# Kernel optimization log

Measured on AMD Instinct MI355X. Metric: run time of the kernel, lower is better.

## Reference

```python
import jax, jax.numpy as jnp
import numpy as np
from jax import lax

D = 512      # inter_dim
E = 768      # expand_dim
S = 256      # squeeze_dim
BUCKET = 64
N_BLOCK = 6

def layernorm(x, g, b, eps):
    m = jnp.mean(x, axis=-1, keepdims=True)
    v = jnp.mean(jnp.square(x - m), axis=-1, keepdims=True)
    return (x - m) / jnp.sqrt(v + eps) * g + b

def setup_inputs():
    key = jax.random.key(0)
    ks = jax.random.split(key, 12)
    B, N, IN = 4, 4096, 768
    def rn(k, shape, scale):
        return jax.random.normal(k, shape, dtype=jnp.float32) * scale
    return {
        "xs": jax.random.normal(ks[0], (B, N, IN), dtype=jnp.float32),
        # in1: Linear(IN, D) + LayerNorm(eps=1e-8) + LeakyReLU(0.1)
        "W_in": rn(ks[1], (IN, D), IN ** -0.5), "b_in": jnp.zeros(D),
        "ln_in_g": jnp.ones(D), "ln_in_b": jnp.zeros(D),
        # 6 GAU (FlashQuadAttention) blocks, params stacked on leading axis
        "blk_ln_g": jnp.ones((N_BLOCK, D)), "blk_ln_b": jnp.zeros((N_BLOCK, D)),
        "blk_Wuv": rn(ks[2], (N_BLOCK, D, 2 * E + S), D ** -0.5),
        "blk_buv": jnp.zeros((N_BLOCK, 2 * E + S)),
        "blk_gamma": jnp.ones((N_BLOCK, 2, S)) + rn(ks[3], (N_BLOCK, 2, S), 0.02),
        "blk_beta": rn(ks[4], (N_BLOCK, 2, S), 0.02),
        "blk_Wo": rn(ks[5], (N_BLOCK, E, D), E ** -0.5),
        "blk_bo": jnp.zeros((N_BLOCK, D)),
        # tr_layer (applied inside tree loop)
        "tr_W": rn(ks[6], (D, D), D ** -0.5), "tr_b": jnp.zeros(D),
        "tr_a": jnp.full((), 1e-6, dtype=jnp.float32),
        # out1 = TransLayer + Linear(D, out_dim)
        "tr2_W": rn(ks[7], (D, D), D ** -0.5), "tr2_b": jnp.zeros(D),
        "tr2_a": jnp.full((), 1e-6, dtype=jnp.float32),
        "out_W": rn(ks[8], (D, 2), D ** -0.5), "out_b": jnp.zeros(2),
    }

def reference(xs, W_in, b_in, ln_in_g, ln_in_b,
              blk_ln_g, blk_ln_b, blk_Wuv, blk_buv, blk_gamma, blk_beta,
              blk_Wo, blk_bo, tr_W, tr_b, tr_a, tr2_W, tr2_b, tr2_a,
              out_W, out_b):
    def subnet(h):  # h: [n_buckets, BUCKET, D]
        def step(h, p):
            lg, lb, Wuv, buv, gam, bet, Wo, bo = p
            n = layernorm(h, lg, lb, 1e-5)
            uvb = jax.nn.silu(n @ Wuv + buv)
            u, v, base = uvb[..., :E], uvb[..., E:2 * E], uvb[..., 2 * E:]
            q = base * gam[0] + bet[0]
            k = base * gam[1] + bet[1]
            Lq = h.shape[1]
            a = jnp.square(jax.nn.relu(jnp.einsum('gls,gms->glm', q, k) / Lq))
            o = jnp.einsum('glm,gme->gle', a, v) * u
            return h + o @ Wo + bo, None
        h, _ = lax.scan(step, h, (blk_ln_g, blk_ln_b, blk_Wuv, blk_buv,
                                  blk_gamma, blk_beta, blk_Wo, blk_bo))
        return h

    def tr_layer(x, W, b, a):
        return x + jax.nn.gelu(x @ W + b, approximate=False) * a

    def run_sample(x):  # x: [N, in_dim]
        h = layernorm(x @ W_in + b_in, ln_in_g, ln_in_b, 1e-8)
        h = jnp.where(h > 0, h, 0.1 * h)  # LeakyReLU(0.1)
        seq = h
        ys = []
        while seq.shape[0] > 1:  # static shapes -> unrolled tree levels
            ids = jnp.argsort(jnp.linalg.norm(seq, axis=-1))  # sort by L2 norm
            buckets = seq[ids].reshape(-1, BUCKET, D)
            gy = subnet(buckets).mean(axis=1)           # [n_buckets, D]
            ys.append(tr_layer(gy, tr_W, tr_b, tr_a).mean(axis=0))
            seq = gy
        return jnp.stack(ys, 0).mean(0)  # [D]

    y = jax.vmap(run_sample)(xs)          # [B, D]
    y = tr_layer(y, tr2_W, tr2_b, tr2_a)  # out1 TransLayer
    return y @ out_W + out_b              # [B, out_dim]
```

## Files before the change

### kernel.cpp

```cpp
#include <hip/hip_runtime.h>
#include <math.h>

#define R1C 16384

enum { OP_STORE = 0, OP_SILU = 1, OP_RESID = 2, OP_TR = 3 };

typedef _Float16 f16x8 __attribute__((ext_vector_type(8)));
typedef float f32x4 __attribute__((ext_vector_type(4)));

__device__ __forceinline__ float silu_f(float x) { return x / (1.0f + __expf(-x)); }
__device__ __forceinline__ float gelu_f(float x) {
  return 0.5f * x * (1.0f + erff(x * 0.70710678118654752f));
}

__device__ __forceinline__ void gll16(const void* g, const void* l) {
  __builtin_amdgcn_global_load_lds(
      (const __attribute__((address_space(1))) unsigned int*)g,
      (__attribute__((address_space(3))) unsigned int*)l, 16, 0, 0);
}


__global__ __launch_bounds__(256) void gemm_f16(
    const _Float16* __restrict__ A, int lda,
    const _Float16* __restrict__ Bt, int ldb,
    float* __restrict__ C, int ldc, int K,
    const float* __restrict__ bias, int mode,
    const int* __restrict__ ids)
{
  const int BUF = 128 * 32;
  __shared__ _Float16 As[2 * BUF];
  __shared__ _Float16 Bs[2 * BUF];
  int tid = threadIdx.x;
  int lane = tid & 63, w = tid >> 6;
  int wm = w >> 1, wn = w & 1;
  int row0 = blockIdx.y * 128, col0 = blockIdx.x * 128;

  int p0 = w * 64 + lane;
  int p1 = 256 + w * 64 + lane;
  int m0 = p0 >> 2, k0e = (((p0 & 3) - (m0 >> 1)) & 3) * 8;
  int m1 = p1 >> 2, k1e = (((p1 & 3) - (m1 >> 1)) & 3) * 8;
  const _Float16* gA0 = A + (size_t)(row0 + m0) * lda + k0e;
  const _Float16* gA1 = A + (size_t)(row0 + m1) * lda + k1e;
  const _Float16* gB0 = Bt + (size_t)(col0 + m0) * ldb + k0e;
  const _Float16* gB1 = Bt + (size_t)(col0 + m1) * ldb + k1e;
  const _Float16* lA0 = As + (size_t)(w * 64) * 8;
  const _Float16* lA1 = As + (size_t)(256 + w * 64) * 8;
  const _Float16* lB0 = Bs + (size_t)(w * 64) * 8;
  const _Float16* lB1 = Bs + (size_t)(256 + w * 64) * 8;

  int mrow = lane & 15, quad = lane >> 4;
  const f16x8* aptr[4];
  const f16x8* bptr[4];
#pragma unroll
  for (int t = 0; t < 4; ++t) {
    int ml = wm * 64 + t * 16 + mrow;
    aptr[t] = (const f16x8*)(As + (size_t)(ml * 4 + ((quad + (ml >> 1)) & 3)) * 8);
    int nl = wn * 64 + t * 16 + mrow;
    bptr[t] = (const f16x8*)(Bs + (size_t)(nl * 4 + ((quad + (nl >> 1)) & 3)) * 8);
  }

  f32x4 acc[4][4] = {};

  gll16(gA0, lA0); gll16(gA1, lA1);
  gll16(gB0, lB0); gll16(gB1, lB1);
  gA0 += 32; gA1 += 32; gB0 += 32; gB1 += 32;

  for (int kt = 0; kt < K; kt += 32) {
    int cur = (kt >> 5) & 1;
    __syncthreads();
    if (kt + 32 < K) {
      int nx = cur ^ 1;
      gll16(gA0, lA0 + nx * BUF); gll16(gA1, lA1 + nx * BUF);
      gll16(gB0, lB0 + nx * BUF); gll16(gB1, lB1 + nx * BUF);
      gA0 += 32; gA1 += 32; gB0 += 32; gB1 += 32;
    }
    int fo = cur * (BUF / 8);
    f16x8 af[4], bfr[4];
#pragma unroll
    for (int t = 0; t < 4; ++t) { af[t] = *(aptr[t] + fo); bfr[t] = *(bptr[t] + fo); }
#pragma unroll
    for (int mt = 0; mt < 4; ++mt)
#pragma unroll
      for (int nt = 0; nt < 4; ++nt)
        acc[mt][nt] = __builtin_amdgcn_mfma_f32_16x16x32_f16(
            af[mt], bfr[nt], acc[mt][nt], 0, 0, 0);
  }

#pragma unroll
  for (int mt = 0; mt < 4; ++mt) {
#pragma unroll
    for (int nt = 0; nt < 4; ++nt) {
      int c = col0 + wn * 64 + nt * 16 + mrow;
      float bv = bias ? bias[c] : 0.0f;
#pragma unroll
      for (int reg = 0; reg < 4; ++reg) {
        int r = row0 + wm * 64 + mt * 16 + quad * 4 + reg;
        float val = acc[mt][nt][reg] + bv;
        if (mode == OP_STORE) {
          C[(size_t)r * ldc + c] = val;
        } else if (mode == OP_SILU) {
          C[(size_t)r * ldc + c] = silu_f(val);
        } else {
          int hr = ids ? ids[r] : r;
          C[(size_t)hr * ldc + c] += val;
        }
      }
    }
  }
}

__global__ __launch_bounds__(256) void gemm_f16_split(
    const _Float16* __restrict__ Ah, const _Float16* __restrict__ Al, int lda,
    const _Float16* __restrict__ Bh, const _Float16* __restrict__ Bl, int ldb,
    float* __restrict__ C, int ldc, int K, const float* __restrict__ bias)
{
  const int BUF = 128 * 32;
  __shared__ _Float16 AsH[2 * BUF], AsL[2 * BUF];
  __shared__ _Float16 BsH[2 * BUF], BsL[2 * BUF];
  int tid = threadIdx.x;
  int lane = tid & 63, w = tid >> 6;
  int wm = w >> 1, wn = w & 1;
  int row0 = blockIdx.y * 128, col0 = blockIdx.x * 128;

  int p0 = w * 64 + lane;
  int p1 = 256 + w * 64 + lane;
  int m0 = p0 >> 2, k0e = (((p0 & 3) - (m0 >> 1)) & 3) * 8;
  int m1 = p1 >> 2, k1e = (((p1 & 3) - (m1 >> 1)) & 3) * 8;
  size_t a0 = (size_t)(row0 + m0) * lda + k0e;
  size_t a1 = (size_t)(row0 + m1) * lda + k1e;
  size_t b0 = (size_t)(col0 + m0) * ldb + k0e;
  size_t b1 = (size_t)(col0 + m1) * ldb + k1e;
  size_t l0 = (size_t)(w * 64) * 8;
  size_t l1 = (size_t)(256 + w * 64) * 8;

  int mrow = lane & 15, quad = lane >> 4;
  size_t aoff[4], boff[4];
#pragma unroll
  for (int t = 0; t < 4; ++t) {
    int ml = wm * 64 + t * 16 + mrow;
    aoff[t] = (size_t)(ml * 4 + ((quad + (ml >> 1)) & 3)) * 8;
    int nl = wn * 64 + t * 16 + mrow;
    boff[t] = (size_t)(nl * 4 + ((quad + (nl >> 1)) & 3)) * 8;
  }

  f32x4 acc[4][4] = {};

  gll16(Ah + a0, AsH + l0); gll16(Ah + a1, AsH + l1);
  gll16(Al + a0, AsL + l0); gll16(Al + a1, AsL + l1);
  gll16(Bh + b0, BsH + l0); gll16(Bh + b1, BsH + l1);
  gll16(Bl + b0, BsL + l0); gll16(Bl + b1, BsL + l1);
  a0 += 32; a1 += 32; b0 += 32; b1 += 32;

  for (int kt = 0; kt < K; kt += 32) {
    int cur = (kt >> 5) & 1;
    __syncthreads();
    if (kt + 32 < K) {
      int nx = cur ^ 1;
      size_t o = (size_t)nx * BUF;
      gll16(Ah + a0, AsH + l0 + o); gll16(Ah + a1, AsH + l1 + o);
      gll16(Al + a0, AsL + l0 + o); gll16(Al + a1, AsL + l1 + o);
      gll16(Bh + b0, BsH + l0 + o); gll16(Bh + b1, BsH + l1 + o);
      gll16(Bl + b0, BsL + l0 + o); gll16(Bl + b1, BsL + l1 + o);
      a0 += 32; a1 += 32; b0 += 32; b1 += 32;
    }
    size_t o = (size_t)cur * BUF;
    f16x8 ah[4], al_[4], bh[4], bl[4];
#pragma unroll
    for (int t = 0; t < 4; ++t) {
      ah[t]  = *(const f16x8*)(AsH + aoff[t] + o);
      al_[t] = *(const f16x8*)(AsL + aoff[t] + o);
      bh[t]  = *(const f16x8*)(BsH + boff[t] + o);
      bl[t]  = *(const f16x8*)(BsL + boff[t] + o);
    }
#pragma unroll
    for (int mt = 0; mt < 4; ++mt)
#pragma unroll
      for (int nt = 0; nt < 4; ++nt) {
        acc[mt][nt] = __builtin_amdgcn_mfma_f32_16x16x32_f16(
            ah[mt], bh[nt], acc[mt][nt], 0, 0, 0);
        acc[mt][nt] = __builtin_amdgcn_mfma_f32_16x16x32_f16(
            ah[mt], bl[nt], acc[mt][nt], 0, 0, 0);
        acc[mt][nt] = __builtin_amdgcn_mfma_f32_16x16x32_f16(
            al_[mt], bh[nt], acc[mt][nt], 0, 0, 0);
      }
  }

#pragma unroll
  for (int mt = 0; mt < 4; ++mt)
#pragma unroll
    for (int nt = 0; nt < 4; ++nt) {
      int c = col0 + wn * 64 + nt * 16 + mrow;
      float bv = bias ? bias[c] : 0.0f;
#pragma unroll
      for (int reg = 0; reg < 4; ++reg) {
        int r = row0 + wm * 64 + mt * 16 + quad * 4 + reg;
        C[(size_t)r * ldc + c] = acc[mt][nt][reg] + bv;
      }
    }
}

__global__ __launch_bounds__(256) void gemm_f16_uvb(
    const _Float16* __restrict__ A, int lda,
    const _Float16* __restrict__ Bt,
    int c0, int nu,
    _Float16* __restrict__ ub, _Float16* __restrict__ vb, float* __restrict__ baseb,
    int CH, int K, const float* __restrict__ buv)
{
  const int BUF = 128 * 32;
  __shared__ _Float16 As[2 * BUF];
  __shared__ _Float16 Bs[2 * BUF];
  int tid = threadIdx.x;
  int lane = tid & 63, w = tid >> 6;
  int wm = w >> 1, wn = w & 1;
  int row0 = blockIdx.y * 128;

  int x = blockIdx.x;
  int xl, regbase, ldc_, is_base = 0;
  _Float16* dst16 = nullptr;
  if (x < nu)            { xl = x;          regbase = c0;        dst16 = ub; ldc_ = CH; }
  else if (x < 2 * nu)   { xl = x - nu;     regbase = 768 + c0;  dst16 = vb; ldc_ = CH; }
  else                   { xl = x - 2 * nu; regbase = 1536;      is_base = 1; ldc_ = 256; }
  int brow0 = regbase + xl * 128;
  int dcol0 = xl * 128;

  int p0 = w * 64 + lane;
  int p1 = 256 + w * 64 + lane;
  int m0 = p0 >> 2, k0e = (((p0 & 3) - (m0 >> 1)) & 3) * 8;
  int m1 = p1 >> 2, k1e = (((p1 & 3) - (m1 >> 1)) & 3) * 8;
  const _Float16* gA0 = A + (size_t)(row0 + m0) * lda + k0e;
  const _Float16* gA1 = A + (size_t)(row0 + m1) * lda + k1e;
  const _Float16* gB0 = Bt + (size_t)(brow0 + m0) * 512 + k0e;
  const _Float16* gB1 = Bt + (size_t)(brow0 + m1) * 512 + k1e;
  const _Float16* lA0 = As + (size_t)(w * 64) * 8;
  const _Float16* lA1 = As + (size_t)(256 + w * 64) * 8;
  const _Float16* lB0 = Bs + (size_t)(w * 64) * 8;
  const _Float16* lB1 = Bs + (size_t)(256 + w * 64) * 8;

  int mrow = lane & 15, quad = lane >> 4;
  const f16x8* aptr[4];
  const f16x8* bptr[4];
#pragma unroll
  for (int t = 0; t < 4; ++t) {
    int ml = wm * 64 + t * 16 + mrow;
    aptr[t] = (const f16x8*)(As + (size_t)(ml * 4 + ((quad + (ml >> 1)) & 3)) * 8);
    int nl = wn * 64 + t * 16 + mrow;
    bptr[t] = (const f16x8*)(Bs + (size_t)(nl * 4 + ((quad + (nl >> 1)) & 3)) * 8);
  }

  f32x4 acc[4][4] = {};

  gll16(gA0, lA0); gll16(gA1, lA1);
  gll16(gB0, lB0); gll16(gB1, lB1);
  gA0 += 32; gA1 += 32; gB0 += 32; gB1 += 32;

  for (int kt = 0; kt < K; kt += 32) {
    int cur = (kt >> 5) & 1;
    __syncthreads();
    if (kt + 32 < K) {
      int nx = cur ^ 1;
      gll16(gA0, lA0 + nx * BUF); gll16(gA1, lA1 + nx * BUF);
      gll16(gB0, lB0 + nx * BUF); gll16(gB1, lB1 + nx * BUF);
      gA0 += 32; gA1 += 32; gB0 += 32; gB1 += 32;
    }
    int fo = cur * (BUF / 8);
    f16x8 af[4], bfr[4];
#pragma unroll
    for (int t = 0; t < 4; ++t) { af[t] = *(aptr[t] + fo); bfr[t] = *(bptr[t] + fo); }
#pragma unroll
    for (int mt = 0; mt < 4; ++mt)
#pragma unroll
      for (int nt = 0; nt < 4; ++nt)
        acc[mt][nt] = __builtin_amdgcn_mfma_f32_16x16x32_f16(
            af[mt], bfr[nt], acc[mt][nt], 0, 0, 0);
  }

#pragma unroll
  for (int mt = 0; mt < 4; ++mt) {
#pragma unroll
    for (int nt = 0; nt < 4; ++nt) {
      int lc = wn * 64 + nt * 16 + mrow;
      float bv = buv[brow0 + lc];
#pragma unroll
      for (int reg = 0; reg < 4; ++reg) {
        int r = row0 + wm * 64 + mt * 16 + quad * 4 + reg;
        float val = silu_f(acc[mt][nt][reg] + bv);
        if (is_base) baseb[(size_t)r * 256 + dcol0 + lc] = val;
        else         dst16[(size_t)r * ldc_ + dcol0 + lc] = (_Float16)val;
      }
    }
  }
}

__global__ __launch_bounds__(256) void attnapply_fused(
    const float* __restrict__ base, const float* __restrict__ gb,
    const float* __restrict__ bb, const _Float16* __restrict__ v,
    const _Float16* __restrict__ u, _Float16* __restrict__ t, int CH)
{
  __shared__ _Float16 smem[3 * 64 * 72];
  _Float16* qs = smem;
  _Float16* ks = smem + 64 * 72;
  _Float16* al = smem + 2 * 64 * 72;
  _Float16* vT = smem;

  int g = blockIdx.x, tid = threadIdx.x;
  int lane = tid & 63, w = tid >> 6;
  int mrow = lane & 15, quad = lane >> 4;
  int srow = tid >> 2, scol = (tid & 3) * 16;

  f32x4 acc[4] = {};
  for (int s0 = 0; s0 < 256; s0 += 64) {
    const float* bp = base + ((size_t)g * 64 + srow) * 256 + s0 + scol;
#pragma unroll
    for (int j4 = 0; j4 < 4; ++j4) {
      float4 xv = *(const float4*)(bp + j4 * 4);
      float xx[4] = {xv.x, xv.y, xv.z, xv.w};
#pragma unroll
      for (int j = 0; j < 4; ++j) {
        int s = s0 + scol + j4 * 4 + j;
        qs[srow * 72 + scol + j4 * 4 + j] = (_Float16)(xx[j] * gb[s] + bb[s]);
        ks[srow * 72 + scol + j4 * 4 + j] = (_Float16)(xx[j] * gb[256 + s] + bb[256 + s]);
      }
    }
    __syncthreads();
#pragma unroll
    for (int ks2 = 0; ks2 < 2; ++ks2) {
      f16x8 aq = *(const f16x8*)(qs + (w * 16 + mrow) * 72 + ks2 * 32 + quad * 8);
#pragma unroll
      for (int nt = 0; nt < 4; ++nt) {
        f16x8 bk = *(const f16x8*)(ks + (nt * 16 + mrow) * 72 + ks2 * 32 + quad * 8);
        acc[nt] = __builtin_amdgcn_mfma_f32_16x16x32_f16(aq, bk, acc[nt], 0, 0, 0);
      }
    }
    __syncthreads();
  }
#pragma unroll
  for (int nt = 0; nt < 4; ++nt)
#pragma unroll
    for (int reg = 0; reg < 4; ++reg) {
      float val = acc[nt][reg] * (1.0f / 64.0f);
      val = val > 0.0f ? val : 0.0f;
      val = val * val;
      al[(w * 16 + quad * 4 + reg) * 72 + nt * 16 + mrow] = (_Float16)val;
    }
  __syncthreads();

  for (int e0 = 0; e0 < CH; e0 += 64) {
    const _Float16* vp = v + ((size_t)g * 64 + srow) * CH + e0 + scol;
    f16x8 x0 = *(const f16x8*)vp;
    f16x8 x1 = *(const f16x8*)(vp + 8);
#pragma unroll
    for (int j = 0; j < 8; ++j) {
      vT[(scol + j) * 72 + srow] = x0[j];
      vT[(scol + 8 + j) * 72 + srow] = x1[j];
    }
    __syncthreads();
    f32x4 acc2[4] = {};
#pragma unroll
    for (int ks2 = 0; ks2 < 2; ++ks2) {
      f16x8 af = *(const f16x8*)(al + (w * 16 + mrow) * 72 + ks2 * 32 + quad * 8);
#pragma unroll
      for (int nt = 0; nt < 4; ++nt) {
        f16x8 bf = *(const f16x8*)(vT + (nt * 16 + mrow) * 72 + ks2 * 32 + quad * 8);
        acc2[nt] = __builtin_amdgcn_mfma_f32_16x16x32_f16(af, bf, acc2[nt], 0, 0, 0);
      }
    }
#pragma unroll
    for (int nt = 0; nt < 4; ++nt)
#pragma unroll
      for (int reg = 0; reg < 4; ++reg) {
        int row = w * 16 + quad * 4 + reg;
        int col = e0 + nt * 16 + mrow;
        size_t idx = ((size_t)g * 64 + row) * CH + col;
        t[idx] = (_Float16)(acc2[nt][reg] * (float)u[idx]);
      }
    __syncthreads();
  }
}

__global__ __launch_bounds__(256) void gemm_f32(
    const float* __restrict__ A, int lda,
    const float* __restrict__ B, int ldb,
    float* __restrict__ C, int ldc,
    int M, int N, int K,
    const float* __restrict__ bias, int mode,
    const int* __restrict__ ids,
    const float* __restrict__ X,
    const float* __restrict__ alpha)
{
  __shared__ float As[16][68];
  __shared__ float Bs[16][68];
  int tid = threadIdx.x;
  int tx = tid & 15, ty = tid >> 4;
  int col0 = blockIdx.x * 64, row0 = blockIdx.y * 64;
  float acc[4][4] = {};
  int arow = tid >> 2;
  int ak   = (tid & 3) * 4;
  int bk   = tid >> 4;
  int bn   = (tid & 15) * 4;

  for (int kt = 0; kt < K; kt += 16) {
    float4 av = make_float4(0.f, 0.f, 0.f, 0.f);
    if (row0 + arow < M)
      av = *(const float4*)&A[(size_t)(row0 + arow) * lda + kt + ak];
    As[ak + 0][arow] = av.x; As[ak + 1][arow] = av.y;
    As[ak + 2][arow] = av.z; As[ak + 3][arow] = av.w;
    float4 bv = *(const float4*)&B[(size_t)(kt + bk) * ldb + col0 + bn];
    *(float4*)&Bs[bk][bn] = bv;
    __syncthreads();
#pragma unroll
    for (int k = 0; k < 16; ++k) {
      const float4 a4 = *(const float4*)&As[k][ty * 4];
      const float4 b4 = *(const float4*)&Bs[k][tx * 4];
      float a_[4] = {a4.x, a4.y, a4.z, a4.w};
      float b_[4] = {b4.x, b4.y, b4.z, b4.w};
#pragma unroll
      for (int i = 0; i < 4; ++i)
#pragma unroll
        for (int j = 0; j < 4; ++j)
          acc[i][j] = fmaf(a_[i], b_[j], acc[i][j]);
    }
    __syncthreads();
  }

#pragma unroll
  for (int i = 0; i < 4; ++i) {
    int r = row0 + ty * 4 + i;
    if (r >= M) continue;
#pragma unroll
    for (int j = 0; j < 4; ++j) {
      int c = col0 + tx * 4 + j;
      float val = acc[i][j] + (bias ? bias[c] : 0.0f);
      if (mode == OP_STORE) {
        C[(size_t)r * ldc + c] = val;
      } else if (mode == OP_SILU) {
        C[(size_t)r * ldc + c] = silu_f(val);
      } else if (mode == OP_RESID) {
        int hr = ids ? ids[r] : r;
        C[(size_t)hr * ldc + c] += val;
      } else {
        C[(size_t)r * ldc + c] = X[(size_t)r * ldc + c] + gelu_f(val) * alpha[0];
      }
    }
  }
}

__global__ __launch_bounds__(256) void transpose_cast(
    const float* __restrict__ in, _Float16* __restrict__ out, int K, int N)
{
  in  += (size_t)blockIdx.z * K * N;
  out += (size_t)blockIdx.z * K * N;
  __shared__ float t[32][33];
  int k0 = blockIdx.y * 32, n0 = blockIdx.x * 32;
  int tx = threadIdx.x & 31, ty = threadIdx.x >> 5;
  for (int i = ty; i < 32; i += 8) {
    int k = k0 + i, n = n0 + tx;
    t[i][tx] = (k < K && n < N) ? in[(size_t)k * N + n] : 0.0f;
  }
  __syncthreads();
  for (int i = ty; i < 32; i += 8) {
    int n = n0 + i, k = k0 + tx;
    if (n < N && k < K) out[(size_t)n * K + k] = (_Float16)t[tx][i];
  }
}

__global__ __launch_bounds__(256) void transpose_split(
    const float* __restrict__ in, _Float16* __restrict__ hi,
    _Float16* __restrict__ lo, int K, int N)
{
  __shared__ float t[32][33];
  int k0 = blockIdx.y * 32, n0 = blockIdx.x * 32;
  int tx = threadIdx.x & 31, ty = threadIdx.x >> 5;
  for (int i = ty; i < 32; i += 8) {
    int k = k0 + i, n = n0 + tx;
    t[i][tx] = (k < K && n < N) ? in[(size_t)k * N + n] : 0.0f;
  }
  __syncthreads();
  for (int i = ty; i < 32; i += 8) {
    int n = n0 + i, k = k0 + tx;
    if (n < N && k < K) {
      float x = t[tx][i];
      _Float16 h = (_Float16)x;
      hi[(size_t)n * K + k] = h;
      lo[(size_t)n * K + k] = (_Float16)(x - (float)h);
    }
  }
}

__global__ __launch_bounds__(256) void split_f16_kernel(
    const float* __restrict__ in, _Float16* __restrict__ hi,
    _Float16* __restrict__ lo, int n)
{
  int i = blockIdx.x * 256 + threadIdx.x;
  if (i < n) {
    float x = in[i];
    _Float16 h = (_Float16)x;
    hi[i] = h;
    lo[i] = (_Float16)(x - (float)h);
  }
}

template <typename OUT>
__global__ __launch_bounds__(256) void ln_kernel(
    const float* __restrict__ src, const int* __restrict__ ids,
    OUT* __restrict__ dst, const float* __restrict__ g,
    const float* __restrict__ b, float eps, int leaky,
    float* __restrict__ nrm2)
{
  int r = blockIdx.x;
  int sr = ids ? ids[r] : r;
  int tid = threadIdx.x;
  float v0 = src[(size_t)sr * 512 + tid];
  float v1 = src[(size_t)sr * 512 + tid + 256];
  __shared__ float red[256], red2[256];
  red[tid] = v0 + v1;
  red2[tid] = v0 * v0 + v1 * v1;
  __syncthreads();
  for (int s = 128; s > 0; s >>= 1) {
    if (tid < s) { red[tid] += red[tid + s]; red2[tid] += red2[tid + s]; }
    __syncthreads();
  }
  float mean = red[0] * (1.0f / 512.0f);
  float var  = red2[0] * (1.0f / 512.0f) - mean * mean;
  float rs = rsqrtf(var + eps);
  float o0 = (v0 - mean) * rs * g[tid] + b[tid];
  float o1 = (v1 - mean) * rs * g[tid + 256] + b[tid + 256];
  if (leaky) {
    o0 = o0 > 0.0f ? o0 : 0.1f * o0;
    o1 = o1 > 0.0f ? o1 : 0.1f * o1;
  }
  dst[(size_t)r * 512 + tid] = (OUT)o0;
  dst[(size_t)r * 512 + tid + 256] = (OUT)o1;
  if (nrm2) {
    __syncthreads();
    red[tid] = o0 * o0 + o1 * o1;
    __syncthreads();
    for (int s = 128; s > 0; s >>= 1) {
      if (tid < s) red[tid] += red[tid + s];
      __syncthreads();
    }
    if (tid == 0) nrm2[r] = red[0];
  }
}

__global__ __launch_bounds__(128) void permute_rows(
    const float* __restrict__ src, const int* __restrict__ ids,
    float* __restrict__ dst)
{
  int r = blockIdx.x, sr = ids[r];
  const float4* s = (const float4*)(src + (size_t)sr * 512);
  float4* d = (float4*)(dst + (size_t)r * 512);
  d[threadIdx.x] = s[threadIdx.x];
}

__global__ __launch_bounds__(1024) void sort_kernel(const float* __restrict__ norm2,
                                                    int* __restrict__ ids)
{
  __shared__ float key[4096];
  __shared__ int   val[4096];
  int s = blockIdx.x, tid = threadIdx.x;
  for (int i = tid; i < 4096; i += 1024) { key[i] = norm2[s * 4096 + i]; val[i] = i; }
  __syncthreads();
  for (int len = 2; len <= 4096; len <<= 1) {
    for (int j = len >> 1; j > 0; j >>= 1) {
      for (int t = tid; t < 2048; t += 1024) {
        int i1 = (t << 1) - (t & (j - 1));
        int i2 = i1 + j;
        bool up = ((i1 & len) == 0);
        float ka = key[i1], kb = key[i2];
        int va = val[i1], vb = val[i2];
        bool gt = (ka > kb) || (ka == kb && va > vb);
        if (gt == up) {
          key[i1] = kb; key[i2] = ka;
          val[i1] = vb; val[i2] = va;
        }
      }
      __syncthreads();
    }
  }
  for (int i = tid; i < 4096; i += 1024) ids[s * 4096 + i] = s * 4096 + val[i];
}

__global__ __launch_bounds__(256) void bucketmean_kernel(
    const float* __restrict__ src, const int* __restrict__ ids,
    float* __restrict__ dst)
{
  int g = blockIdx.x, tid = threadIdx.x;
  float s0 = 0.0f, s1 = 0.0f;
  for (int i = 0; i < 64; ++i) {
    int r = g * 64 + i;
    if (ids) r = ids[r];
    s0 += src[(size_t)r * 512 + tid];
    s1 += src[(size_t)r * 512 + tid + 256];
  }
  dst[(size_t)g * 512 + tid] = s0 * (1.0f / 64.0f);
  dst[(size_t)g * 512 + tid + 256] = s1 * (1.0f / 64.0f);
}

__global__ void avg_kernel(const float* __restrict__ a, const float* __restrict__ b,
                           float* __restrict__ o, int n)
{
  int i = blockIdx.x * 256 + threadIdx.x;
  if (i < n) o[i] = 0.5f * (a[i] + b[i]);
}

__global__ void out_kernel(const float* __restrict__ y, const float* __restrict__ W,
                           const float* __restrict__ b, float* __restrict__ out)
{
  int tid = threadIdx.x;
  if (tid < 8) {
    int s = tid >> 1, j = tid & 1;
    float acc = b[j];
    for (int d = 0; d < 512; ++d) acc += y[s * 512 + d] * W[d * 2 + j];
    out[s * 2 + j] = acc;
  }
}

extern "C" void kernel_launch(void* const* d_in, const int* in_sizes, int n_in,
                              void* d_out, int out_size, void* d_ws, size_t ws_size,
                              hipStream_t stream)
{
  const float* xs       = (const float*)d_in[0];
  const float* W_in     = (const float*)d_in[1];
  const float* b_in     = (const float*)d_in[2];
  const float* ln_in_g  = (const float*)d_in[3];
  const float* ln_in_b  = (const float*)d_in[4];
  const float* blk_ln_g = (const float*)d_in[5];
  const float* blk_ln_b = (const float*)d_in[6];
  const float* blk_Wuv  = (const float*)d_in[7];
  const float* blk_buv  = (const float*)d_in[8];
  const float* blk_gam  = (const float*)d_in[9];
  const float* blk_bet  = (const float*)d_in[10];
  const float* blk_Wo   = (const float*)d_in[11];
  const float* blk_bo   = (const float*)d_in[12];
  const float* tr_W     = (const float*)d_in[13];
  const float* tr_b     = (const float*)d_in[14];
  const float* tr_a     = (const float*)d_in[15];
  const float* tr2_W    = (const float*)d_in[16];
  const float* tr2_b    = (const float*)d_in[17];
  const float* tr2_a    = (const float*)d_in[18];
  const float* out_W    = (const float*)d_in[19];
  const float* out_b    = (const float*)d_in[20];
  float* outp = (float*)d_out;

  const size_t R1 = R1C;

  char* wsb = (char*)d_ws;
  size_t off = 0;
  auto carve = [&](size_t bytes) {
    char* r = wsb + off;
    off = (off + bytes + 255) & ~(size_t)255;
    return (void*)r;
  };
  float* h      = (float*)carve(R1 * 512 * 4);
  float* hslot  = (float*)carve(R1 * 512 * 4);
  float* norm2b = (float*)carve(R1 * 4);
  int*   idsb   = (int*)carve(R1 * 4);
  float* gy     = (float*)carve((size_t)256 * 512 * 4);
  float* tl     = (float*)carve((size_t)256 * 512 * 4);
  float* gy2    = (float*)carve(4 * 512 * 4);
  float* ys0    = (float*)carve(4 * 512 * 4);
  float* ys1    = (float*)carve(4 * 512 * 4);
  float* yv     = (float*)carve(4 * 512 * 4);
  float* y2     = (float*)carve(4 * 512 * 4);
  _Float16* Wuvt = (_Float16*)carve((size_t)6 * 1792 * 512 * 2);
  _Float16* Wot  = (_Float16*)carve((size_t)6 * 512 * 768 * 2);
  size_t persistent = off;

  size_t stageA_sorted = 2 * R1 * 768 * 2 + 2 * (size_t)512 * 768 * 2 + R1 * 512 * 4 + 2048;
  size_t block768 = R1 * 256 * 4 + 3 * R1 * (size_t)768 * 2 + 2048;
  size_t un_sorted = stageA_sorted > block768 ? stageA_sorted : block768;
  bool sorted_mode = (persistent + un_sorted + 4096 <= ws_size);

  int CH = 768;
  bool splitA = true;
  if (!sorted_mode) {
    size_t stageA_fb = 2 * R1 * 768 * 2 + 2 * (size_t)512 * 768 * 2 + 1024;
    auto block_bytes = [&](size_t ch) {
      return R1 * 256 * 4 + 3 * R1 * ch * 2 + 2048;
    };
    CH = 0; splitA = false;
    const int cand[4] = {768, 384, 256, 128};
    for (int ci = 0; ci < 4; ++ci) {
      size_t bb2 = block_bytes(cand[ci]);
      size_t un2 = bb2 > stageA_fb ? bb2 : stageA_fb;
      if (persistent + un2 + 4096 <= ws_size) { CH = cand[ci]; splitA = true; break; }
    }
    if (!CH) {
      for (int ci = 0; ci < 4; ++ci)
        if (persistent + block_bytes(cand[ci]) + 4096 <= ws_size) { CH = cand[ci]; break; }
      if (!CH) CH = 128;
    }
  }
  int nu = CH / 128;

  char* un = wsb + ((persistent + 255) & ~(size_t)255);
  _Float16* xs_hi = (_Float16*)un;
  _Float16* xs_lo = xs_hi + R1 * 768;
  _Float16* Wt_hi = xs_lo + R1 * 768;
  _Float16* Wt_lo = Wt_hi + (size_t)512 * 768;
  float*    nbA   = sorted_mode ? (float*)(Wt_lo + (size_t)512 * 768) : hslot;
  float*    baseb = (float*)un;
  _Float16* ub    = (_Float16*)(un + R1 * 256 * 4);
  _Float16* vb    = ub + R1 * (size_t)CH;
  _Float16* tb    = vb + R1 * (size_t)CH;
  _Float16* nbuf  = sorted_mode ? tb : (_Float16*)hslot;
  float* hres = sorted_mode ? hslot : h;
  const int* blkids = sorted_mode ? nullptr : idsb;

  dim3 blk(256);

  transpose_cast<<<dim3(56, 16, 6), blk, 0, stream>>>(blk_Wuv, Wuvt, 512, 1792);
  transpose_cast<<<dim3(16, 24, 6), blk, 0, stream>>>(blk_Wo, Wot, 768, 512);

  if (splitA) {
    split_f16_kernel<<<(int)(R1 * 768 / 256), blk, 0, stream>>>(xs, xs_hi, xs_lo,
                                                                (int)(R1 * 768));
    transpose_split<<<dim3(16, 24, 1), blk, 0, stream>>>(W_in, Wt_hi, Wt_lo, 768, 512);
    gemm_f16_split<<<dim3(4, 128), blk, 0, stream>>>(xs_hi, xs_lo, 768,
        Wt_hi, Wt_lo, 768, nbA, 512, 768, b_in);
  } else {
    gemm_f32<<<dim3(8, 256), blk, 0, stream>>>(xs, 768, W_in, 512, nbA, 512,
        16384, 512, 768, b_in, OP_STORE, nullptr, nullptr, nullptr);
  }
  ln_kernel<float><<<16384, 256, 0, stream>>>(nbA, nullptr, h, ln_in_g, ln_in_b,
                                              1e-8f, 1, norm2b);
  sort_kernel<<<4, 1024, 0, stream>>>(norm2b, idsb);
  if (sorted_mode)
    permute_rows<<<16384, 128, 0, stream>>>(h, idsb, hres);

  for (int b = 0; b < 6; ++b) {
    const _Float16* Wuv_t = Wuvt + (size_t)b * 1792 * 512;
    const float*    buv   = blk_buv + b * 1792;
    const _Float16* Wo_t  = Wot + (size_t)b * 512 * 768;
    ln_kernel<_Float16><<<16384, 256, 0, stream>>>(hres, blkids, nbuf,
        blk_ln_g + b * 512, blk_ln_b + b * 512, 1e-5f, 0, nullptr);
    for (int c0 = 0; c0 < 768; c0 += CH) {
      int incl = (c0 == 0) ? 2 : 0;
      gemm_f16_uvb<<<dim3(2 * nu + incl, 128), blk, 0, stream>>>(nbuf, 512, Wuv_t,
          c0, nu, ub, vb, baseb, CH, 512, buv);
      attnapply_fused<<<256, 256, 0, stream>>>(baseb, blk_gam + b * 512,
          blk_bet + b * 512, vb, ub, tb, CH);
      const float* bo = (c0 + CH == 768) ? (blk_bo + b * 512) : nullptr;
      gemm_f16<<<dim3(4, 128), blk, 0, stream>>>(tb, CH, Wo_t + c0, 768,
          hres, 512, CH, bo, OP_RESID, blkids);
    }
  }
  bucketmean_kernel<<<256, 256, 0, stream>>>(hres, blkids, gy);

  gemm_f32<<<dim3(8, 4), blk, 0, stream>>>(gy, 512, tr_W, 512, tl, 512,
      256, 512, 512, tr_b, OP_TR, nullptr, gy, tr_a);
  bucketmean_kernel<<<4, 256, 0, stream>>>(tl, nullptr, ys0);

  for (int b = 0; b < 6; ++b) {
    const _Float16* Wuv_t = Wuvt + (size_t)b * 1792 * 512;
    const float*    buv   = blk_buv + b * 1792;
    const _Float16* Wo_t  = Wot + (size_t)b * 512 * 768;
    ln_kernel<_Float16><<<256, 256, 0, stream>>>(gy, nullptr, nbuf, blk_ln_g + b * 512,
                                                 blk_ln_b + b * 512, 1e-5f, 0, nullptr);
    for (int c0 = 0; c0 < 768; c0 += CH) {
      int incl = (c0 == 0) ? 2 : 0;
      gemm_f16_uvb<<<dim3(2 * nu + incl, 2), blk, 0, stream>>>(nbuf, 512, Wuv_t,
          c0, nu, ub, vb, baseb, CH, 512, buv);
      attnapply_fused<<<4, 256, 0, stream>>>(baseb, blk_gam + b * 512,
          blk_bet + b * 512, vb, ub, tb, CH);
      const float* bo = (c0 + CH == 768) ? (blk_bo + b * 512) : nullptr;
      gemm_f16<<<dim3(4, 2), blk, 0, stream>>>(tb, CH, Wo_t + c0, 768,
          gy, 512, CH, bo, OP_RESID, nullptr);
    }
  }
  bucketmean_kernel<<<4, 256, 0, stream>>>(gy, nullptr, gy2);

  gemm_f32<<<dim3(8, 1), blk, 0, stream>>>(gy2, 512, tr_W, 512, ys1, 512,
      4, 512, 512, tr_b, OP_TR, nullptr, gy2, tr_a);
  avg_kernel<<<8, 256, 0, stream>>>(ys0, ys1, yv, 2048);
  gemm_f32<<<dim3(8, 1), blk, 0, stream>>>(yv, 512, tr2_W, 512, y2, 512,
      4, 512, 512, tr2_b, OP_TR, nullptr, yv, tr2_a);
  out_kernel<<<1, 64, 0, stream>>>(y2, out_W, out_b, outp);
}
```

Measured before the change: 1.798 ms.

## Use 512-thread GEMM blocks and split attention-apply across expand chunks

The three f16 MFMA GEMM kernels now launch 512 threads (8 waves) per 128x128 tile. Each wave computes a 32x64 sub-tile, so each thread issues one global-to-LDS load per operand instead of two and holds half as many accumulators. The attention-apply kernel gains a second grid dimension that splits the expand channels into chunks of up to 256, giving more blocks per bucket. The aim is more waves in flight and more parallelism, at the cost of redundant q/k/score recomputation per chunk and more barrier participants per block.

```diff
diff --git a/kernel.cpp b/kernel.cpp
--- a/kernel.cpp
+++ b/kernel.cpp
@@ -20,7 +20,7 @@
 }
 
 
-__global__ __launch_bounds__(256) void gemm_f16(
+__global__ __launch_bounds__(512) void gemm_f16(
     const _Float16* __restrict__ A, int lda,
     const _Float16* __restrict__ Bt, int ldb,
     float* __restrict__ C, int ldc, int K,
@@ -35,51 +35,48 @@
   int wm = w >> 1, wn = w & 1;
   int row0 = blockIdx.y * 128, col0 = blockIdx.x * 128;
 
-  int p0 = w * 64 + lane;
-  int p1 = 256 + w * 64 + lane;
-  int m0 = p0 >> 2, k0e = (((p0 & 3) - (m0 >> 1)) & 3) * 8;
-  int m1 = p1 >> 2, k1e = (((p1 & 3) - (m1 >> 1)) & 3) * 8;
+  int m0 = tid >> 2;
+  int k0e = (((tid & 3) - (m0 >> 1)) & 3) * 8;
   const _Float16* gA0 = A + (size_t)(row0 + m0) * lda + k0e;
-  const _Float16* gA1 = A + (size_t)(row0 + m1) * lda + k1e;
   const _Float16* gB0 = Bt + (size_t)(col0 + m0) * ldb + k0e;
-  const _Float16* gB1 = Bt + (size_t)(col0 + m1) * ldb + k1e;
   const _Float16* lA0 = As + (size_t)(w * 64) * 8;
-  const _Float16* lA1 = As + (size_t)(256 + w * 64) * 8;
   const _Float16* lB0 = Bs + (size_t)(w * 64) * 8;
-  const _Float16* lB1 = Bs + (size_t)(256 + w * 64) * 8;
 
   int mrow = lane & 15, quad = lane >> 4;
-  const f16x8* aptr[4];
+  const f16x8* aptr[2];
   const f16x8* bptr[4];
 #pragma unroll
-  for (int t = 0; t < 4; ++t) {
-    int ml = wm * 64 + t * 16 + mrow;
+  for (int t = 0; t < 2; ++t) {
+    int ml = wm * 32 + t * 16 + mrow;
     aptr[t] = (const f16x8*)(As + (size_t)(ml * 4 + ((quad + (ml >> 1)) & 3)) * 8);
-    int nl = wn * 64 + t * 16 + mrow;
-    bptr[t] = (const f16x8*)(Bs + (size_t)(nl * 4 + ((quad + (nl >> 1)) & 3)) * 8);
-  }
-
-  f32x4 acc[4][4] = {};
-
-  gll16(gA0, lA0); gll16(gA1, lA1);
-  gll16(gB0, lB0); gll16(gB1, lB1);
-  gA0 += 32; gA1 += 32; gB0 += 32; gB1 += 32;
+  }
+#pragma unroll
+  for (int nt = 0; nt < 4; ++nt) {
+    int nl = wn * 64 + nt * 16 + mrow;
+    bptr[nt] = (const f16x8*)(Bs + (size_t)(nl * 4 + ((quad + (nl >> 1)) & 3)) * 8);
+  }
+
+  f32x4 acc[2][4] = {};
+
+  gll16(gA0, lA0); gll16(gB0, lB0);
+  gA0 += 32; gB0 += 32;
 
   for (int kt = 0; kt < K; kt += 32) {
     int cur = (kt >> 5) & 1;
     __syncthreads();
     if (kt + 32 < K) {
       int nx = cur ^ 1;
-      gll16(gA0, lA0 + nx * BUF); gll16(gA1, lA1 + nx * BUF);
-      gll16(gB0, lB0 + nx * BUF); gll16(gB1, lB1 + nx * BUF);
-      gA0 += 32; gA1 += 32; gB0 += 32; gB1 += 32;
+      gll16(gA0, lA0 + nx * BUF); gll16(gB0, lB0 + nx * BUF);
+      gA0 += 32; gB0 += 32;
     }
     int fo = cur * (BUF / 8);
-    f16x8 af[4], bfr[4];
-#pragma unroll
-    for (int t = 0; t < 4; ++t) { af[t] = *(aptr[t] + fo); bfr[t] = *(bptr[t] + fo); }
-#pragma unroll
-    for (int mt = 0; mt < 4; ++mt)
+    f16x8 af[2], bfr[4];
+#pragma unroll
+    for (int t = 0; t < 2; ++t) af[t] = *(aptr[t] + fo);
+#pragma unroll
+    for (int nt = 0; nt < 4; ++nt) bfr[nt] = *(bptr[nt] + fo);
+#pragma unroll
+    for (int mt = 0; mt < 2; ++mt)
 #pragma unroll
       for (int nt = 0; nt < 4; ++nt)
         acc[mt][nt] = __builtin_amdgcn_mfma_f32_16x16x32_f16(
@@ -87,14 +84,14 @@
   }
 
 #pragma unroll
-  for (int mt = 0; mt < 4; ++mt) {
+  for (int mt = 0; mt < 2; ++mt) {
 #pragma unroll
     for (int nt = 0; nt < 4; ++nt) {
       int c = col0 + wn * 64 + nt * 16 + mrow;
       float bv = bias ? bias[c] : 0.0f;
 #pragma unroll
       for (int reg = 0; reg < 4; ++reg) {
-        int r = row0 + wm * 64 + mt * 16 + quad * 4 + reg;
+        int r = row0 + wm * 32 + mt * 16 + quad * 4 + reg;
         float val = acc[mt][nt][reg] + bv;
         if (mode == OP_STORE) {
           C[(size_t)r * ldc + c] = val;
@@ -109,7 +106,7 @@
   }
 }
 
-__global__ __launch_bounds__(256) void gemm_f16_split(
+__global__ __launch_bounds__(512) void gemm_f16_split(
     const _Float16* __restrict__ Ah, const _Float16* __restrict__ Al, int lda,
     const _Float16* __restrict__ Bh, const _Float16* __restrict__ Bl, int ldb,
     float* __restrict__ C, int ldc, int K, const float* __restrict__ bias)
@@ -122,58 +119,54 @@
   int wm = w >> 1, wn = w & 1;
   int row0 = blockIdx.y * 128, col0 = blockIdx.x * 128;
 
-  int p0 = w * 64 + lane;
-  int p1 = 256 + w * 64 + lane;
-  int m0 = p0 >> 2, k0e = (((p0 & 3) - (m0 >> 1)) & 3) * 8;
-  int m1 = p1 >> 2, k1e = (((p1 & 3) - (m1 >> 1)) & 3) * 8;
+  int m0 = tid >> 2;
+  int k0e = (((tid & 3) - (m0 >> 1)) & 3) * 8;
   size_t a0 = (size_t)(row0 + m0) * lda + k0e;
-  size_t a1 = (size_t)(row0 + m1) * lda + k1e;
   size_t b0 = (size_t)(col0 + m0) * ldb + k0e;
-  size_t b1 = (size_t)(col0 + m1) * ldb + k1e;
   size_t l0 = (size_t)(w * 64) * 8;
-  size_t l1 = (size_t)(256 + w * 64) * 8;
 
   int mrow = lane & 15, quad = lane >> 4;
-  size_t aoff[4], boff[4];
-#pragma unroll
-  for (int t = 0; t < 4; ++t) {
-    int ml = wm * 64 + t * 16 + mrow;
+  size_t aoff[2], boff[4];
+#pragma unroll
+  for (int t = 0; t < 2; ++t) {
+    int ml = wm * 32 + t * 16 + mrow;
     aoff[t] = (size_t)(ml * 4 + ((quad + (ml >> 1)) & 3)) * 8;
-    int nl = wn * 64 + t * 16 + mrow;
-    boff[t] = (size_t)(nl * 4 + ((quad + (nl >> 1)) & 3)) * 8;
-  }
-
-  f32x4 acc[4][4] = {};
-
-  gll16(Ah + a0, AsH + l0); gll16(Ah + a1, AsH + l1);
-  gll16(Al + a0, AsL + l0); gll16(Al + a1, AsL + l1);
-  gll16(Bh + b0, BsH + l0); gll16(Bh + b1, BsH + l1);
-  gll16(Bl + b0, BsL + l0); gll16(Bl + b1, BsL + l1);
-  a0 += 32; a1 += 32; b0 += 32; b1 += 32;
+  }
+#pragma unroll
+  for (int nt = 0; nt < 4; ++nt) {
+    int nl = wn * 64 + nt * 16 + mrow;
+    boff[nt] = (size_t)(nl * 4 + ((quad + (nl >> 1)) & 3)) * 8;
+  }
+
+  f32x4 acc[2][4] = {};
+
+  gll16(Ah + a0, AsH + l0); gll16(Al + a0, AsL + l0);
+  gll16(Bh + b0, BsH + l0); gll16(Bl + b0, BsL + l0);
+  a0 += 32; b0 += 32;
 
   for (int kt = 0; kt < K; kt += 32) {
     int cur = (kt >> 5) & 1;
     __syncthreads();
     if (kt + 32 < K) {
-      int nx = cur ^ 1;
-      size_t o = (size_t)nx * BUF;
-      gll16(Ah + a0, AsH + l0 + o); gll16(Ah + a1, AsH + l1 + o);
-      gll16(Al + a0, AsL + l0 + o); gll16(Al + a1, AsL + l1 + o);
-      gll16(Bh + b0, BsH + l0 + o); gll16(Bh + b1, BsH + l1 + o);
-      gll16(Bl + b0, BsL + l0 + o); gll16(Bl + b1, BsL + l1 + o);
-      a0 += 32; a1 += 32; b0 += 32; b1 += 32;
+      size_t o = (size_t)(cur ^ 1) * BUF;
+      gll16(Ah + a0, AsH + l0 + o); gll16(Al + a0, AsL + l0 + o);
+      gll16(Bh + b0, BsH + l0 + o); gll16(Bl + b0, BsL + l0 + o);
+      a0 += 32; b0 += 32;
     }
     size_t o = (size_t)cur * BUF;
-    f16x8 ah[4], al_[4], bh[4], bl[4];
-#pragma unroll
-    for (int t = 0; t < 4; ++t) {
+    f16x8 ah[2], al_[2], bh[4], bl[4];
+#pragma unroll
+    for (int t = 0; t < 2; ++t) {
       ah[t]  = *(const f16x8*)(AsH + aoff[t] + o);
       al_[t] = *(const f16x8*)(AsL + aoff[t] + o);
-      bh[t]  = *(const f16x8*)(BsH + boff[t] + o);
-      bl[t]  = *(const f16x8*)(BsL + boff[t] + o);
-    }
-#pragma unroll
-    for (int mt = 0; mt < 4; ++mt)
+    }
+#pragma unroll
+    for (int nt = 0; nt < 4; ++nt) {
+      bh[nt] = *(const f16x8*)(BsH + boff[nt] + o);
+      bl[nt] = *(const f16x8*)(BsL + boff[nt] + o);
+    }
+#pragma unroll
+    for (int mt = 0; mt < 2; ++mt)
 #pragma unroll
       for (int nt = 0; nt < 4; ++nt) {
         acc[mt][nt] = __builtin_amdgcn_mfma_f32_16x16x32_f16(
@@ -186,20 +179,20 @@
   }
 
 #pragma unroll
-  for (int mt = 0; mt < 4; ++mt)
+  for (int mt = 0; mt < 2; ++mt)
 #pragma unroll
     for (int nt = 0; nt < 4; ++nt) {
       int c = col0 + wn * 64 + nt * 16 + mrow;
       float bv = bias ? bias[c] : 0.0f;
 #pragma unroll
       for (int reg = 0; reg < 4; ++reg) {
-        int r = row0 + wm * 64 + mt * 16 + quad * 4 + reg;
+        int r = row0 + wm * 32 + mt * 16 + quad * 4 + reg;
         C[(size_t)r * ldc + c] = acc[mt][nt][reg] + bv;
       }
     }
 }
 
-__global__ __launch_bounds__(256) void gemm_f16_uvb(
+__global__ __launch_bounds__(512) void gemm_f16_uvb(
     const _Float16* __restrict__ A, int lda,
     const _Float16* __restrict__ Bt,
     int c0, int nu,
@@ -223,51 +216,48 @@
   int brow0 = regbase + xl * 128;
   int dcol0 = xl * 128;
 
-  int p0 = w * 64 + lane;
-  int p1 = 256 + w * 64 + lane;
-  int m0 = p0 >> 2, k0e = (((p0 & 3) - (m0 >> 1)) & 3) * 8;
-  int m1 = p1 >> 2, k1e = (((p1 & 3) - (m1 >> 1)) & 3) * 8;
+  int m0 = tid >> 2;
+  int k0e = (((tid & 3) - (m0 >> 1)) & 3) * 8;
   const _Float16* gA0 = A + (size_t)(row0 + m0) * lda + k0e;
-  const _Float16* gA1 = A + (size_t)(row0 + m1) * lda + k1e;
   const _Float16* gB0 = Bt + (size_t)(brow0 + m0) * 512 + k0e;
-  const _Float16* gB1 = Bt + (size_t)(brow0 + m1) * 512 + k1e;
   const _Float16* lA0 = As + (size_t)(w * 64) * 8;
-  const _Float16* lA1 = As + (size_t)(256 + w * 64) * 8;
   const _Float16* lB0 = Bs + (size_t)(w * 64) * 8;
-  const _Float16* lB1 = Bs + (size_t)(256 + w * 64) * 8;
 
   int mrow = lane & 15, quad = lane >> 4;
-  const f16x8* aptr[4];
+  const f16x8* aptr[2];
   const f16x8* bptr[4];
 #pragma unroll
-  for (int t = 0; t < 4; ++t) {
-    int ml = wm * 64 + t * 16 + mrow;
+  for (int t = 0; t < 2; ++t) {
+    int ml = wm * 32 + t * 16 + mrow;
     aptr[t] = (const f16x8*)(As + (size_t)(ml * 4 + ((quad + (ml >> 1)) & 3)) * 8);
-    int nl = wn * 64 + t * 16 + mrow;
-    bptr[t] = (const f16x8*)(Bs + (size_t)(nl * 4 + ((quad + (nl >> 1)) & 3)) * 8);
-  }
-
-  f32x4 acc[4][4] = {};
-
-  gll16(gA0, lA0); gll16(gA1, lA1);
-  gll16(gB0, lB0); gll16(gB1, lB1);
-  gA0 += 32; gA1 += 32; gB0 += 32; gB1 += 32;
+  }
+#pragma unroll
+  for (int nt = 0; nt < 4; ++nt) {
+    int nl = wn * 64 + nt * 16 + mrow;
+    bptr[nt] = (const f16x8*)(Bs + (size_t)(nl * 4 + ((quad + (nl >> 1)) & 3)) * 8);
+  }
+
+  f32x4 acc[2][4] = {};
+
+  gll16(gA0, lA0); gll16(gB0, lB0);
+  gA0 += 32; gB0 += 32;
 
   for (int kt = 0; kt < K; kt += 32) {
     int cur = (kt >> 5) & 1;
     __syncthreads();
     if (kt + 32 < K) {
       int nx = cur ^ 1;
-      gll16(gA0, lA0 + nx * BUF); gll16(gA1, lA1 + nx * BUF);
-      gll16(gB0, lB0 + nx * BUF); gll16(gB1, lB1 + nx * BUF);
-      gA0 += 32; gA1 += 32; gB0 += 32; gB1 += 32;
+      gll16(gA0, lA0 + nx * BUF); gll16(gB0, lB0 + nx * BUF);
+      gA0 += 32; gB0 += 32;
     }
     int fo = cur * (BUF / 8);
-    f16x8 af[4], bfr[4];
-#pragma unroll
-    for (int t = 0; t < 4; ++t) { af[t] = *(aptr[t] + fo); bfr[t] = *(bptr[t] + fo); }
-#pragma unroll
-    for (int mt = 0; mt < 4; ++mt)
+    f16x8 af[2], bfr[4];
+#pragma unroll
+    for (int t = 0; t < 2; ++t) af[t] = *(aptr[t] + fo);
+#pragma unroll
+    for (int nt = 0; nt < 4; ++nt) bfr[nt] = *(bptr[nt] + fo);
+#pragma unroll
+    for (int mt = 0; mt < 2; ++mt)
 #pragma unroll
       for (int nt = 0; nt < 4; ++nt)
         acc[mt][nt] = __builtin_amdgcn_mfma_f32_16x16x32_f16(
@@ -275,14 +265,14 @@
   }
 
 #pragma unroll
-  for (int mt = 0; mt < 4; ++mt) {
+  for (int mt = 0; mt < 2; ++mt) {
 #pragma unroll
     for (int nt = 0; nt < 4; ++nt) {
       int lc = wn * 64 + nt * 16 + mrow;
       float bv = buv[brow0 + lc];
 #pragma unroll
       for (int reg = 0; reg < 4; ++reg) {
-        int r = row0 + wm * 64 + mt * 16 + quad * 4 + reg;
+        int r = row0 + wm * 32 + mt * 16 + quad * 4 + reg;
         float val = silu_f(acc[mt][nt][reg] + bv);
         if (is_base) baseb[(size_t)r * 256 + dcol0 + lc] = val;
         else         dst16[(size_t)r * ldc_ + dcol0 + lc] = (_Float16)val;
@@ -294,7 +284,7 @@
 __global__ __launch_bounds__(256) void attnapply_fused(
     const float* __restrict__ base, const float* __restrict__ gb,
     const float* __restrict__ bb, const _Float16* __restrict__ v,
-    const _Float16* __restrict__ u, _Float16* __restrict__ t, int CH)
+    const _Float16* __restrict__ u, _Float16* __restrict__ t, int CH, int ech)
 {
   __shared__ _Float16 smem[3 * 64 * 72];
   _Float16* qs = smem;
@@ -302,7 +292,8 @@
   _Float16* al = smem + 2 * 64 * 72;
   _Float16* vT = smem;
 
-  int g = blockIdx.x, tid = threadIdx.x;
+  int g = blockIdx.y, tid = threadIdx.x;
+  int e_lo = blockIdx.x * ech, e_hi = e_lo + ech;
   int lane = tid & 63, w = tid >> 6;
   int mrow = lane & 15, quad = lane >> 4;
   int srow = tid >> 2, scol = (tid & 3) * 16;
@@ -344,7 +335,7 @@
     }
   __syncthreads();
 
-  for (int e0 = 0; e0 < CH; e0 += 64) {
+  for (int e0 = e_lo; e0 < e_hi; e0 += 64) {
     const _Float16* vp = v + ((size_t)g * 64 + srow) * CH + e0 + scol;
     f16x8 x0 = *(const f16x8*)vp;
     f16x8 x1 = *(const f16x8*)(vp + 8);
@@ -692,6 +683,8 @@
     }
   }
   int nu = CH / 128;
+  int ech = CH >= 256 ? 256 : CH;
+  int nch = CH / ech;
 
   char* un = wsb + ((persistent + 255) & ~(size_t)255);
   _Float16* xs_hi = (_Float16*)un;
@@ -708,6 +701,7 @@
   const int* blkids = sorted_mode ? nullptr : idsb;
 
   dim3 blk(256);
+  dim3 blk5(512);
 
   transpose_cast<<<dim3(56, 16, 6), blk, 0, stream>>>(blk_Wuv, Wuvt, 512, 1792);
   transpose_cast<<<dim3(16, 24, 6), blk, 0, stream>>>(blk_Wo, Wot, 768, 512);
@@ -716,7 +710,7 @@
     split_f16_kernel<<<(int)(R1 * 768 / 256), blk, 0, stream>>>(xs, xs_hi, xs_lo,
                                                                 (int)(R1 * 768));
     transpose_split<<<dim3(16, 24, 1), blk, 0, stream>>>(W_in, Wt_hi, Wt_lo, 768, 512);
-    gemm_f16_split<<<dim3(4, 128), blk, 0, stream>>>(xs_hi, xs_lo, 768,
+    gemm_f16_split<<<dim3(4, 128), blk5, 0, stream>>>(xs_hi, xs_lo, 768,
         Wt_hi, Wt_lo, 768, nbA, 512, 768, b_in);
   } else {
     gemm_f32<<<dim3(8, 256), blk, 0, stream>>>(xs, 768, W_in, 512, nbA, 512,
@@ -736,12 +730,12 @@
         blk_ln_g + b * 512, blk_ln_b + b * 512, 1e-5f, 0, nullptr);
     for (int c0 = 0; c0 < 768; c0 += CH) {
       int incl = (c0 == 0) ? 2 : 0;
-      gemm_f16_uvb<<<dim3(2 * nu + incl, 128), blk, 0, stream>>>(nbuf, 512, Wuv_t,
+      gemm_f16_uvb<<<dim3(2 * nu + incl, 128), blk5, 0, stream>>>(nbuf, 512, Wuv_t,
           c0, nu, ub, vb, baseb, CH, 512, buv);
-      attnapply_fused<<<256, 256, 0, stream>>>(baseb, blk_gam + b * 512,
-          blk_bet + b * 512, vb, ub, tb, CH);
+      attnapply_fused<<<dim3(nch, 256), blk, 0, stream>>>(baseb, blk_gam + b * 512,
+          blk_bet + b * 512, vb, ub, tb, CH, ech);
       const float* bo = (c0 + CH == 768) ? (blk_bo + b * 512) : nullptr;
-      gemm_f16<<<dim3(4, 128), blk, 0, stream>>>(tb, CH, Wo_t + c0, 768,
+      gemm_f16<<<dim3(4, 128), blk5, 0, stream>>>(tb, CH, Wo_t + c0, 768,
           hres, 512, CH, bo, OP_RESID, blkids);
     }
   }
@@ -759,12 +753,12 @@
                                                  blk_ln_b + b * 512, 1e-5f, 0, nullptr);
     for (int c0 = 0; c0 < 768; c0 += CH) {
       int incl = (c0 == 0) ? 2 : 0;
-      gemm_f16_uvb<<<dim3(2 * nu + incl, 2), blk, 0, stream>>>(nbuf, 512, Wuv_t,
+      gemm_f16_uvb<<<dim3(2 * nu + incl, 2), blk5, 0, stream>>>(nbuf, 512, Wuv_t,
           c0, nu, ub, vb, baseb, CH, 512, buv);
-      attnapply_fused<<<4, 256, 0, stream>>>(baseb, blk_gam + b * 512,
-          blk_bet + b * 512, vb, ub, tb, CH);
+      attnapply_fused<<<dim3(nch, 4), blk, 0, stream>>>(baseb, blk_gam + b * 512,
+          blk_bet + b * 512, vb, ub, tb, CH, ech);
       const float* bo = (c0 + CH == 768) ? (blk_bo + b * 512) : nullptr;
-      gemm_f16<<<dim3(4, 2), blk, 0, stream>>>(tb, CH, Wo_t + c0, 768,
+      gemm_f16<<<dim3(4, 2), blk5, 0, stream>>>(tb, CH, Wo_t + c0, 768,
           gy, 512, CH, bo, OP_RESID, nullptr);
     }
   }
```

After: 1.612 ms. -10.3%, faster.
